# Kernel tuning notes

Measured on AMD Instinct MI355X. Metric: run time of the kernel, lower is better.

## Reference

```python
import jax, jax.numpy as jnp
import numpy as np

B, N, C, H = 8, 4096, 768, 8
EPS = 1e-12  # F.normalize eps


def setup_inputs() -> dict:
    key = jax.random.key(0)
    ks = jax.random.split(key, 4)
    x = jax.random.normal(ks[0], (B, N, C), dtype=jnp.float32)
    w_qkv = jax.random.normal(ks[1], (3 * C, C), dtype=jnp.float32) * 0.02
    temperature = jnp.ones((H, 1, 1), dtype=jnp.float32)
    w_proj = jax.random.normal(ks[2], (C, C), dtype=jnp.float32) * 0.02
    b_proj = jnp.zeros((C,), dtype=jnp.float32)
    return {"x": x, "w_qkv": w_qkv, "temperature": temperature,
            "w_proj": w_proj, "b_proj": b_proj}


def _l2norm(t):
    # F.normalize(t, dim=-1): t / max(||t||_2, eps)
    n = jnp.sqrt(jnp.sum(t * t, axis=-1, keepdims=True))
    return t / jnp.maximum(n, EPS)


def reference(x, w_qkv, temperature, w_proj, b_proj):
    b, n, c = x.shape
    h = H
    hd = c // h
    # qkv projection: (B,N,3C) -> (3,B,H,hd,N)
    qkv = (x @ w_qkv.T).reshape(b, n, 3, h, hd)
    qkv = jnp.transpose(qkv, (2, 0, 3, 4, 1))
    q, k, v = qkv[0], qkv[1], qkv[2]          # each (B,H,hd,N)
    qn = _l2norm(q)                            # normalize over N (token) dim
    kn = _l2norm(k)
    # small per-head covariance attention: (B,H,hd,hd)
    attn = jnp.einsum('bhdn,bhen->bhde', qn, kn) * temperature
    attn = jax.nn.softmax(attn, axis=-1)
    out = jnp.einsum('bhde,bhen->bhdn', attn, v)  # (B,H,hd,N)
    out = jnp.transpose(out, (0, 3, 1, 2)).reshape(b, n, c)
    return out @ w_proj.T + b_proj
```

## Files before the change

### kernel.cpp

```cpp
#include <hip/hip_runtime.h>
#include <cstdint>
#include <cstddef>

#define B_ 8
#define N_ 4096
#define C_ 768
#define H_ 8
#define HD_ 96
#define EPSN 1e-12f
#define NS_ 4

typedef short s16x8 __attribute__((ext_vector_type(8)));
typedef short s16x4 __attribute__((ext_vector_type(4)));
typedef float f32x4 __attribute__((ext_vector_type(4)));

static __device__ __forceinline__ short f2bf(float f) {
  unsigned u = __float_as_uint(f);
  unsigned r = (u + 0x7fff + ((u >> 16) & 1)) >> 16;
  return (short)r;
}
static __device__ __forceinline__ float bf2f(unsigned short s) {
  return __uint_as_float(((unsigned)s) << 16);
}
static __device__ __forceinline__ s16x8 pack8(const float4 a, const float4 b) {
  s16x8 r;
  r[0] = f2bf(a.x); r[1] = f2bf(a.y); r[2] = f2bf(a.z); r[3] = f2bf(a.w);
  r[4] = f2bf(b.x); r[5] = f2bf(b.y); r[6] = f2bf(b.z); r[7] = f2bf(b.w);
  return r;
}

#define TSW(ch, t) ((t) ^ ((((ch) >> 2) & 7) << 3))

static __device__ __forceinline__ int swz(int s) {
  return s ^ (((s >> 7) & 3) << 3);
}

static __device__ __forceinline__ void gld16(const short* g, short* l) {
  __builtin_amdgcn_global_load_lds(
      (const __attribute__((address_space(1))) void*)g,
      (__attribute__((address_space(3))) void*)l, 16, 0, 0);
}

__global__ __launch_bounds__(256)
void xcvt(const float* __restrict__ x, short* __restrict__ xb) {
  const int n8 = (B_ * N_ * C_) / 8;
  for (int i = blockIdx.x * 256 + threadIdx.x; i < n8; i += gridDim.x * 256) {
    const float4 a = *(const float4*)(x + (size_t)i * 8);
    const float4 b = *(const float4*)(x + (size_t)i * 8 + 4);
    *(s16x8*)(xb + (size_t)i * 8) = pack8(a, b);
  }
}

__global__ __launch_bounds__(256)
void wcvt(const float* __restrict__ w, short* __restrict__ wb) {
  const int i = blockIdx.x * 256 + threadIdx.x;
  const float4 a = *(const float4*)(w + (size_t)i * 8);
  const float4 b = *(const float4*)(w + (size_t)i * 8 + 4);
  *(s16x8*)(wb + (size_t)i * 8) = pack8(a, b);
}

template<int BF>
__global__ __launch_bounds__(256)
void gram_p(const float* __restrict__ x, const short* __restrict__ xb,
            float* __restrict__ Gp) {
  const int f = blockIdx.x;
  const int xcd = f & 7;
  const int t = f >> 3;
  const int pair = t % 21;
  const int cdiv = t / 21;
  const int c = xcd + 8 * cdiv;
  const int split = c & 3;
  const int b = c >> 2;

  int rem = pair, ti = 0;
#pragma unroll
  for (int it = 0; it < 5; ++it)
    if (rem >= 6 - ti) { rem -= 6 - ti; ++ti; }
  const int tj = ti + rem;
  const int i0 = ti * 128, j0 = tj * 128;
  const bool diag = (ti == tj);

  const int tid = threadIdx.x;
  const int lane = tid & 63, wave = tid >> 6;
  const int l15 = lane & 15, quad = lane >> 4;
  const int wm = wave & 1, wn = wave >> 1;

  __shared__ __align__(16) short smem[2 * 128 * 72];
  short* At = smem;
  short* Bt = smem + 128 * 72;

  const int tg = tid >> 4;
  const int cg = tid & 15;
  const int t0 = tg * 4;
  const int c0 = cg * 4;
  const float* xbF = x + (size_t)b * N_ * C_;
  const short* xbB = xb + (size_t)b * N_ * C_;

  f32x4 acc[4][4] = {};

  const int nbeg = split * (N_ / NS_);
  const int nend = nbeg + (N_ / NS_);
  for (int n0 = nbeg; n0 < nend; n0 += 64) {
    if (BF) {
      s16x8 la[4], lb[4];
#pragma unroll
      for (int r = 0; r < 4; ++r)
        la[r] = *(const s16x8*)(xbB + (size_t)(n0 + t0 + r) * C_ + i0 + cg * 8);
      if (!diag) {
#pragma unroll
        for (int r = 0; r < 4; ++r)
          lb[r] = *(const s16x8*)(xbB + (size_t)(n0 + t0 + r) * C_ + j0 + cg * 8);
      }
      __syncthreads();
#pragma unroll
      for (int cc = 0; cc < 8; ++cc) {
        const int ch = cg * 8 + cc;
        s16x4 v;
        v[0] = la[0][cc]; v[1] = la[1][cc]; v[2] = la[2][cc]; v[3] = la[3][cc];
        *(s16x4*)&At[ch * 72 + TSW(ch, t0)] = v;
      }
      if (!diag) {
#pragma unroll
        for (int cc = 0; cc < 8; ++cc) {
          const int ch = cg * 8 + cc;
          s16x4 v;
          v[0] = lb[0][cc]; v[1] = lb[1][cc]; v[2] = lb[2][cc]; v[3] = lb[3][cc];
          *(s16x4*)&Bt[ch * 72 + TSW(ch, t0)] = v;
        }
      }
      __syncthreads();
    } else {
      float4 la[2][4], lb[2][4];
#pragma unroll
      for (int q = 0; q < 2; ++q)
#pragma unroll
        for (int r = 0; r < 4; ++r)
          la[q][r] = *(const float4*)(xbF + (size_t)(n0 + t0 + r) * C_ + i0 + c0 + q * 64);
      if (!diag) {
#pragma unroll
        for (int q = 0; q < 2; ++q)
#pragma unroll
          for (int r = 0; r < 4; ++r)
            lb[q][r] = *(const float4*)(xbF + (size_t)(n0 + t0 + r) * C_ + j0 + c0 + q * 64);
      }
      __syncthreads();
#pragma unroll
      for (int q = 0; q < 2; ++q)
#pragma unroll
        for (int cc = 0; cc < 4; ++cc) {
          const int ch = c0 + q * 64 + cc;
          s16x4 v;
          v[0] = f2bf(((const float*)&la[q][0])[cc]);
          v[1] = f2bf(((const float*)&la[q][1])[cc]);
          v[2] = f2bf(((const float*)&la[q][2])[cc]);
          v[3] = f2bf(((const float*)&la[q][3])[cc]);
          *(s16x4*)&At[ch * 72 + TSW(ch, t0)] = v;
        }
      if (!diag) {
#pragma unroll
        for (int q = 0; q < 2; ++q)
#pragma unroll
          for (int cc = 0; cc < 4; ++cc) {
            const int ch = c0 + q * 64 + cc;
            s16x4 v;
            v[0] = f2bf(((const float*)&lb[q][0])[cc]);
            v[1] = f2bf(((const float*)&lb[q][1])[cc]);
            v[2] = f2bf(((const float*)&lb[q][2])[cc]);
            v[3] = f2bf(((const float*)&lb[q][3])[cc]);
            *(s16x4*)&Bt[ch * 72 + TSW(ch, t0)] = v;
          }
      }
      __syncthreads();
    }
    const short* Bre = diag ? At : Bt;
#pragma unroll
    for (int ks = 0; ks < 64; ks += 32) {
      s16x8 af[4], bfr[4];
#pragma unroll
      for (int mi = 0; mi < 4; ++mi) {
        const int ch = wm * 64 + mi * 16 + l15;
        af[mi] = *(const s16x8*)&At[ch * 72 + TSW(ch, ks + quad * 8)];
      }
#pragma unroll
      for (int ni = 0; ni < 4; ++ni) {
        const int ch = wn * 64 + ni * 16 + l15;
        bfr[ni] = *(const s16x8*)&Bre[ch * 72 + TSW(ch, ks + quad * 8)];
      }
#pragma unroll
      for (int ni = 0; ni < 4; ++ni)
#pragma unroll
        for (int mi = 0; mi < 4; ++mi)
          acc[mi][ni] = __builtin_amdgcn_mfma_f32_16x16x32_bf16(af[mi], bfr[ni], acc[mi][ni], 0, 0, 0);
    }
  }

  float* Gpb = Gp + (((size_t)b * 21 + pair) * NS_ + split) * (128 * 128);
#pragma unroll
  for (int mi = 0; mi < 4; ++mi)
#pragma unroll
    for (int ni = 0; ni < 4; ++ni) {
      const int ii = wm * 64 + mi * 16 + quad * 4;
      const int jj = wn * 64 + ni * 16 + l15;
#pragma unroll
      for (int r = 0; r < 4; ++r)
        Gpb[(ii + r) * 128 + jj] = acc[mi][ni][r];
    }
}

__global__ __launch_bounds__(256)
void gram_red(const float* __restrict__ Gp, short* __restrict__ G) {
  const int pair = blockIdx.x;
  int rem = pair, ti = 0;
#pragma unroll
  for (int it = 0; it < 5; ++it)
    if (rem >= 6 - ti) { rem -= 6 - ti; ++ti; }
  const int tj = ti + rem;
  const int b = blockIdx.y;
  const int i0 = ti * 128, j0 = tj * 128;
  const bool diag = (ti == tj);
  const int tid = threadIdx.x;

  __shared__ short Ts[128 * 137];

  const float4* P = (const float4*)(Gp + (((size_t)b * 21 + pair) * NS_) * (128 * 128));
  short* Gb = G + (size_t)b * C_ * C_;

#pragma unroll
  for (int it = 0; it < 16; ++it) {
    const int q = tid + it * 256;
    const int row = q >> 5;
    const int c4 = q & 31;
    float4 v = P[q];
    const float4 v1 = P[q + 4096];
    const float4 v2 = P[q + 8192];
    const float4 v3 = P[q + 12288];
    v.x += v1.x + v2.x + v3.x;
    v.y += v1.y + v2.y + v3.y;
    v.z += v1.z + v2.z + v3.z;
    v.w += v1.w + v2.w + v3.w;
    s16x4 sv;
    sv[0] = f2bf(v.x); sv[1] = f2bf(v.y); sv[2] = f2bf(v.z); sv[3] = f2bf(v.w);
    *(s16x4*)&Gb[(size_t)(i0 + row) * C_ + j0 + c4 * 4] = sv;
    if (!diag) {
#pragma unroll
      for (int c = 0; c < 4; ++c)
        Ts[(c4 * 4 + c) * 137 + row] = sv[c];
    }
  }
  if (!diag) {
    __syncthreads();
#pragma unroll
    for (int p = 0; p < 8; ++p) {
      const int id = tid + p * 256;
      const int j = id >> 4, cs = (id & 15) * 8;
      *(s16x8*)&Gb[(size_t)(j0 + j) * C_ + i0 + cs] = *(const s16x8*)&Ts[j * 137 + cs];
    }
  }
}

__global__ __launch_bounds__(256)
void gemm_nt_bf(const short* __restrict__ A, const short* __restrict__ Bb,
                short* __restrict__ Out, size_t sB, size_t sO) {
  const int z = blockIdx.z;
  const int n0 = blockIdx.x * 128;
  const int m0 = blockIdx.y * 128;
  const int tid = threadIdx.x;
  const int lane = tid & 63, wave = tid >> 6;
  const int l15 = lane & 15, quad = lane >> 4;
  const int wm = wave & 1, wn = wave >> 1;

  __shared__ __align__(16) short As[2][128 * 32];
  __shared__ __align__(16) short Bs[2][128 * 32];

  const short* asrc[2]; const short* bsrc[2];
  int doff[2];
#pragma unroll
  for (int cc = 0; cc < 2; ++cc) {
    const int P = wave * 1024 + cc * 512 + lane * 8;
    const int L = swz(P);
    const int row = L >> 5, col = L & 31;
    asrc[cc] = A + (size_t)(m0 + row) * C_ + col;
    bsrc[cc] = Bb + (size_t)z * sB + (size_t)(n0 + row) * C_ + col;
    doff[cc] = wave * 1024 + cc * 512;
  }

  f32x4 acc[4][4] = {};

#pragma unroll
  for (int cc = 0; cc < 2; ++cc) {
    gld16(asrc[cc], &As[0][doff[cc]]);
    gld16(bsrc[cc], &Bs[0][doff[cc]]);
  }
#pragma unroll
  for (int cc = 0; cc < 2; ++cc) {
    gld16(asrc[cc] + 32, &As[1][doff[cc]]);
    gld16(bsrc[cc] + 32, &Bs[1][doff[cc]]);
  }

  int cur = 0;
  const int NT = C_ / 32;
  for (int t = 0; t < NT; ++t) {
    if (t < NT - 1) asm volatile("s_waitcnt vmcnt(4)" ::: "memory");
    else            asm volatile("s_waitcnt vmcnt(0)" ::: "memory");
    __builtin_amdgcn_sched_barrier(0);
    __builtin_amdgcn_s_barrier();
    s16x8 af[4];
#pragma unroll
    for (int mi = 0; mi < 4; ++mi)
      af[mi] = *(const s16x8*)&As[cur][swz((wm * 64 + mi * 16 + l15) * 32 + quad * 8)];
    __builtin_amdgcn_s_setprio(1);
#pragma unroll
    for (int ni = 0; ni < 4; ++ni) {
      const s16x8 bf = *(const s16x8*)&Bs[cur][swz((wn * 64 + ni * 16 + l15) * 32 + quad * 8)];
#pragma unroll
      for (int mi = 0; mi < 4; ++mi)
        acc[mi][ni] = __builtin_amdgcn_mfma_f32_16x16x32_bf16(af[mi], bf, acc[mi][ni], 0, 0, 0);
    }
    __builtin_amdgcn_s_setprio(0);
    __builtin_amdgcn_sched_barrier(0);
    __builtin_amdgcn_s_barrier();
    __builtin_amdgcn_sched_barrier(0);
    if (t + 2 < NT) {
      const int nx = (t + 2) * 32;
#pragma unroll
      for (int cc = 0; cc < 2; ++cc) {
        gld16(asrc[cc] + nx, &As[cur][doff[cc]]);
        gld16(bsrc[cc] + nx, &Bs[cur][doff[cc]]);
      }
    }
    cur ^= 1;
  }

  short* ob = Out + (size_t)z * sO;
#pragma unroll
  for (int mi = 0; mi < 4; ++mi) {
    const int m = m0 + wm * 64 + mi * 16 + quad * 4;
#pragma unroll
    for (int ni = 0; ni < 4; ++ni) {
      const int n = n0 + wn * 64 + ni * 16 + l15;
#pragma unroll
      for (int r = 0; r < 4; ++r)
        ob[(size_t)(m + r) * C_ + n] = f2bf(acc[mi][ni][r]);
    }
  }
}

__global__ __launch_bounds__(256)
void gemm_fb(const float* __restrict__ A, const short* __restrict__ Bb,
             short* __restrict__ Out, size_t sB, size_t sO) {
  const int z = blockIdx.z;
  const int n0 = blockIdx.x * 128;
  const int m0 = blockIdx.y * 128;
  const int tid = threadIdx.x;
  const int lane = tid & 63, wave = tid >> 6;
  const int l15 = lane & 15, quad = lane >> 4;
  const int wm = wave & 1, wn = wave >> 1;

  __shared__ __align__(16) short As[2][128 * 40];
  __shared__ __align__(16) short Bs[2][128 * 32];

  const int ar = tid >> 1;
  const int ak = (tid & 1) * 16;
  const float* ap = A + (size_t)(m0 + ar) * C_ + ak;

  const short* bsrc[2];
  int doff[2];
#pragma unroll
  for (int cc = 0; cc < 2; ++cc) {
    const int P = wave * 1024 + cc * 512 + lane * 8;
    const int L = swz(P);
    bsrc[cc] = Bb + (size_t)z * sB + (size_t)(n0 + (L >> 5)) * C_ + (L & 31);
    doff[cc] = wave * 1024 + cc * 512;
  }

  f32x4 acc[4][4] = {};

  {
    const float4 a0 = *(const float4*)(ap + 0);
    const float4 a1 = *(const float4*)(ap + 4);
    const float4 a2 = *(const float4*)(ap + 8);
    const float4 a3 = *(const float4*)(ap + 12);
#pragma unroll
    for (int cc = 0; cc < 2; ++cc) gld16(bsrc[cc], &Bs[0][doff[cc]]);
    *(s16x8*)&As[0][ar * 40 + ak]     = pack8(a0, a1);
    *(s16x8*)&As[0][ar * 40 + ak + 8] = pack8(a2, a3);
  }
  __syncthreads();
  int cur = 0;
  for (int k0 = 0; k0 < C_; k0 += 32) {
    const int nx = k0 + 32;
    float4 a0, a1, a2, a3;
    if (nx < C_) {
      a0 = *(const float4*)(ap + nx + 0);
      a1 = *(const float4*)(ap + nx + 4);
      a2 = *(const float4*)(ap + nx + 8);
      a3 = *(const float4*)(ap + nx + 12);
#pragma unroll
      for (int cc = 0; cc < 2; ++cc) gld16(bsrc[cc] + nx, &Bs[cur ^ 1][doff[cc]]);
    }
    s16x8 af[4];
#pragma unroll
    for (int mi = 0; mi < 4; ++mi)
      af[mi] = *(const s16x8*)&As[cur][(wm * 64 + mi * 16 + l15) * 40 + quad * 8];
#pragma unroll
    for (int ni = 0; ni < 4; ++ni) {
      const s16x8 bf = *(const s16x8*)&Bs[cur][swz((wn * 64 + ni * 16 + l15) * 32 + quad * 8)];
#pragma unroll
      for (int mi = 0; mi < 4; ++mi)
        acc[mi][ni] = __builtin_amdgcn_mfma_f32_16x16x32_bf16(af[mi], bf, acc[mi][ni], 0, 0, 0);
    }
    if (nx < C_) {
      *(s16x8*)&As[cur ^ 1][ar * 40 + ak]     = pack8(a0, a1);
      *(s16x8*)&As[cur ^ 1][ar * 40 + ak + 8] = pack8(a2, a3);
    }
    __syncthreads();
    cur ^= 1;
  }

  short* ob = Out + (size_t)z * sO;
#pragma unroll
  for (int mi = 0; mi < 4; ++mi) {
    const int m = m0 + wm * 64 + mi * 16 + quad * 4;
#pragma unroll
    for (int ni = 0; ni < 4; ++ni) {
      const int n = n0 + wn * 64 + ni * 16 + l15;
#pragma unroll
      for (int r = 0; r < 4; ++r)
        ob[(size_t)(m + r) * C_ + n] = f2bf(acc[mi][ni][r]);
    }
  }
}

__global__ __launch_bounds__(256)
void row_norms(const short* __restrict__ Y, const float* __restrict__ w_qkv,
               float* __restrict__ norms) {
  const int b = blockIdx.y;
  const int m = blockIdx.x * 4 + (threadIdx.x >> 6);
  const int lane = threadIdx.x & 63;
  const short* y = Y + ((size_t)b * 1536 + m) * C_;
  const float* w = w_qkv + (size_t)m * C_;
  float s = 0.f;
#pragma unroll
  for (int j = 0; j < 3; ++j) {
    const int o = j * 256 + lane * 4;
    const s16x4 yv = *(const s16x4*)(y + o);
    const float4 wv = *(const float4*)(w + o);
    s += bf2f((unsigned short)yv[0]) * wv.x + bf2f((unsigned short)yv[1]) * wv.y +
         bf2f((unsigned short)yv[2]) * wv.z + bf2f((unsigned short)yv[3]) * wv.w;
  }
#pragma unroll
  for (int o = 32; o > 0; o >>= 1) s += __shfl_xor(s, o);
  if (lane == 0) {
    int idx;
    if (m < 768) idx = (b * 8 + m / 96) * 96 + (m % 96);
    else { const int mm = m - 768; idx = B_ * H_ * 96 + (b * 8 + mm / 96) * 96 + (mm % 96); }
    norms[idx] = s;
  }
}

__global__ __launch_bounds__(512)
void s_attn(const short* __restrict__ Y, const short* __restrict__ wb,
            const float* __restrict__ norms, const float* __restrict__ temp,
            float* __restrict__ S) {
  const int bh = blockIdx.x;
  const int b = bh >> 3, h = bh & 7;
  const int tid = threadIdx.x;
  const int lane = tid & 63, wave = tid >> 6;
  const int l15 = lane & 15, quad = lane >> 4;

  __shared__ __align__(16) float Sf[96 * 97];
  __shared__ float qsc[96], ksc[96];
  short* Ys = (short*)Sf;
  short* Ks = (short*)Sf + 96 * 72;

  if (tid < 96)
    qsc[tid] = temp[h] / fmaxf(sqrtf(norms[bh * 96 + tid]), EPSN);
  else if (tid < 192)
    ksc[tid - 96] = 1.0f / fmaxf(sqrtf(norms[B_ * H_ * 96 + bh * 96 + (tid - 96)]), EPSN);

  const short* yb = Y + ((size_t)b * 1536 + h * 96) * C_;
  const short* kb = wb + (size_t)(768 + h * 96) * C_;

  int dts[5], ets[5];
#pragma unroll
  for (int j = 0; j < 5; ++j) {
    const int t = j * 8 + wave;
    dts[j] = t / 6; ets[j] = t % 6;
  }

  f32x4 sc[5] = {};
  const int r0 = tid >> 3, c80 = (tid & 7) * 8;
  const int id1 = tid + 512;
  const int r1 = id1 >> 3, c81 = (id1 & 7) * 8;
  for (int k0 = 0; k0 < C_; k0 += 64) {
    s16x8 yv0, kv0, yv1, kv1;
    yv0 = *(const s16x8*)(yb + (size_t)r0 * C_ + k0 + c80);
    kv0 = *(const s16x8*)(kb + (size_t)r0 * C_ + k0 + c80);
    if (tid < 256) {
      yv1 = *(const s16x8*)(yb + (size_t)r1 * C_ + k0 + c81);
      kv1 = *(const s16x8*)(kb + (size_t)r1 * C_ + k0 + c81);
    }
    __syncthreads();
    *(s16x8*)&Ys[r0 * 72 + c80] = yv0;
    *(s16x8*)&Ks[r0 * 72 + c80] = kv0;
    if (tid < 256) {
      *(s16x8*)&Ys[r1 * 72 + c81] = yv1;
      *(s16x8*)&Ks[r1 * 72 + c81] = kv1;
    }
    __syncthreads();
#pragma unroll
    for (int j = 0; j < 5; ++j) {
      const int t = j * 8 + wave;
      if (t < 36) {
#pragma unroll
        for (int kk = 0; kk < 64; kk += 32) {
          const s16x8 a  = *(const s16x8*)&Ys[(dts[j] * 16 + l15) * 72 + kk + quad * 8];
          const s16x8 bb = *(const s16x8*)&Ks[(ets[j] * 16 + l15) * 72 + kk + quad * 8];
          sc[j] = __builtin_amdgcn_mfma_f32_16x16x32_bf16(a, bb, sc[j], 0, 0, 0);
        }
      }
    }
  }
  __syncthreads();
#pragma unroll
  for (int j = 0; j < 5; ++j) {
    const int t = j * 8 + wave;
    if (t < 36) {
      const int e = ets[j] * 16 + l15;
      const float kf = ksc[e];
#pragma unroll
      for (int r = 0; r < 4; ++r) {
        const int d = dts[j] * 16 + quad * 4 + r;
        Sf[d * 97 + e] = sc[j][r] * qsc[d] * kf;
      }
    }
  }
  __syncthreads();
  float* Sb = S + (size_t)bh * (HD_ * HD_);
  for (int rr = 0; rr < 12; ++rr) {
    const int d = wave * 12 + rr;
    const float v0 = Sf[d * 97 + lane];
    const float v1 = (lane < 32) ? Sf[d * 97 + 64 + lane] : -1e30f;
    float mx = fmaxf(v0, v1);
#pragma unroll
    for (int o = 32; o > 0; o >>= 1) mx = fmaxf(mx, __shfl_xor(mx, o));
    const float e0 = __expf(v0 - mx);
    const float e1 = (lane < 32) ? __expf(v1 - mx) : 0.0f;
    float sum = e0 + e1;
#pragma unroll
    for (int o = 32; o > 0; o >>= 1) sum += __shfl_xor(sum, o);
    const float inv = 1.0f / sum;
    Sb[d * 96 + lane] = e0 * inv;
    if (lane < 32) Sb[d * 96 + 64 + lane] = e1 * inv;
  }
}

__global__ __launch_bounds__(256)
void av_gemm(const float* __restrict__ S, const float* __restrict__ w_qkv,
             short* __restrict__ AVt) {
  const int bh = blockIdx.x;
  const int b = bh >> 3, h = bh & 7;
  const int ct = blockIdx.y * 64;
  const int tid = threadIdx.x;
  __shared__ float at[96 * 97];
  __shared__ float wv[96 * 64];
  const float* Sb = S + (size_t)bh * (HD_ * HD_);
  for (int i = tid; i < 96 * 96; i += 256)
    at[(i / 96) * 97 + (i % 96)] = Sb[i];
  for (int i = tid; i < 96 * 64; i += 256) {
    const int e = i >> 6, c = i & 63;
    wv[e * 64 + c] = w_qkv[(size_t)(2 * C_ + h * 96 + e) * C_ + ct + c];
  }
  __syncthreads();
  const int d0 = (tid >> 4) * 6;
  const int c0 = (tid & 15) * 4;
  float acc[6][4] = {};
  for (int e = 0; e < 96; ++e) {
    const float4 bv = *(const float4*)&wv[e * 64 + c0];
    float aa[6];
#pragma unroll
    for (int i = 0; i < 6; ++i) aa[i] = at[(d0 + i) * 97 + e];
#pragma unroll
    for (int i = 0; i < 6; ++i) {
      acc[i][0] += aa[i] * bv.x; acc[i][1] += aa[i] * bv.y;
      acc[i][2] += aa[i] * bv.z; acc[i][3] += aa[i] * bv.w;
    }
  }
  short* AVb = AVt + (size_t)b * C_ * C_;
#pragma unroll
  for (int i = 0; i < 6; ++i)
#pragma unroll
    for (int j = 0; j < 4; ++j)
      AVb[(size_t)(ct + c0 + j) * C_ + h * 96 + d0 + i] = f2bf(acc[i][j]);
}

__global__ __launch_bounds__(256)
void gemm_xm_bf(const short* __restrict__ xb, const short* __restrict__ Mb,
                const float* __restrict__ bias, float* __restrict__ out) {
  const int f = blockIdx.x;
  const int xcd = f & 7;
  const int t6 = f >> 3;
  const int j6 = t6 % 6;
  const int sdiv = t6 / 6;
  const int s = xcd + 8 * sdiv;
  const int z = s >> 5;
  const int n0 = j6 * 128;
  const int m0 = (s & 31) * 128;
  const int tid = threadIdx.x;
  const int lane = tid & 63;
  const int wave = tid >> 6;
  const int l15 = lane & 15;
  const int quad = lane >> 4;
  const int wm = wave & 1;
  const int wn = wave >> 1;

  __shared__ __align__(16) short As[2][128 * 32];
  __shared__ __align__(16) short Bs[2][128 * 32];

  const short* asrc[2]; const short* bsrc[2];
  int doff[2];
#pragma unroll
  for (int cc = 0; cc < 2; ++cc) {
    const int P = wave * 1024 + cc * 512 + lane * 8;
    const int L = swz(P);
    const int row = L >> 5, col = L & 31;
    asrc[cc] = xb + ((size_t)z * N_ + m0 + row) * C_ + col;
    bsrc[cc] = Mb + (size_t)z * C_ * C_ + (size_t)(n0 + row) * C_ + col;
    doff[cc] = wave * 1024 + cc * 512;
  }

  f32x4 acc[4][4] = {};

#pragma unroll
  for (int cc = 0; cc < 2; ++cc) {
    gld16(asrc[cc], &As[0][doff[cc]]);
    gld16(bsrc[cc], &Bs[0][doff[cc]]);
  }
#pragma unroll
  for (int cc = 0; cc < 2; ++cc) {
    gld16(asrc[cc] + 32, &As[1][doff[cc]]);
    gld16(bsrc[cc] + 32, &Bs[1][doff[cc]]);
  }

  int cur = 0;
  const int NT = C_ / 32;
  for (int t = 0; t < NT; ++t) {
    if (t < NT - 1) asm volatile("s_waitcnt vmcnt(4)" ::: "memory");
    else            asm volatile("s_waitcnt vmcnt(0)" ::: "memory");
    __builtin_amdgcn_sched_barrier(0);
    __builtin_amdgcn_s_barrier();
    s16x8 af[4];
#pragma unroll
    for (int mi = 0; mi < 4; ++mi)
      af[mi] = *(const s16x8*)&As[cur][swz((wm * 64 + mi * 16 + l15) * 32 + quad * 8)];
    __builtin_amdgcn_s_setprio(1);
#pragma unroll
    for (int ni = 0; ni < 4; ++ni) {
      const s16x8 bf = *(const s16x8*)&Bs[cur][swz((wn * 64 + ni * 16 + l15) * 32 + quad * 8)];
#pragma unroll
      for (int mi = 0; mi < 4; ++mi)
        acc[mi][ni] = __builtin_amdgcn_mfma_f32_16x16x32_bf16(af[mi], bf, acc[mi][ni], 0, 0, 0);
    }
    __builtin_amdgcn_s_setprio(0);
    __builtin_amdgcn_sched_barrier(0);
    __builtin_amdgcn_s_barrier();
    __builtin_amdgcn_sched_barrier(0);
    if (t + 2 < NT) {
      const int nx = (t + 2) * 32;
#pragma unroll
      for (int cc = 0; cc < 2; ++cc) {
        gld16(asrc[cc] + nx, &As[cur][doff[cc]]);
        gld16(bsrc[cc] + nx, &Bs[cur][doff[cc]]);
      }
    }
    cur ^= 1;
  }

  float bv[4];
#pragma unroll
  for (int ni = 0; ni < 4; ++ni) bv[ni] = bias[n0 + wn * 64 + ni * 16 + l15];
#pragma unroll
  for (int mi = 0; mi < 4; ++mi) {
    const int m = m0 + wm * 64 + mi * 16 + quad * 4;
#pragma unroll
    for (int ni = 0; ni < 4; ++ni) {
      const int n = n0 + wn * 64 + ni * 16 + l15;
      float* dst = out + ((size_t)z * N_ + m) * C_ + n;
#pragma unroll
      for (int r = 0; r < 4; ++r)
        dst[(size_t)r * C_] = acc[mi][ni][r] + bv[ni];
    }
  }
}

__global__ __launch_bounds__(256)
void gemm_xm_f32(const float* __restrict__ x, const short* __restrict__ Mb,
                 const float* __restrict__ bias, float* __restrict__ out) {
  const int f = blockIdx.x;
  const int xcd = f & 7;
  const int t = f >> 3;
  const int j6 = t % 6;
  const int sdiv = t / 6;
  const int s = xcd + 8 * sdiv;
  const int z = s >> 5;
  const int n0 = j6 * 128;
  const int m0 = (s & 31) * 128;
  const int tid = threadIdx.x;
  const int lane = tid & 63;
  const int wave = tid >> 6;
  const int l15 = lane & 15;
  const int quad = lane >> 4;
  const int wm = wave & 1;
  const int wn = wave >> 1;

  __shared__ __align__(16) short As[128 * 40];
  __shared__ __align__(16) short Bs[128 * 40];

  const int ar = tid >> 1;
  const int ak = (tid & 1) * 16;
  const float* xp = x + ((size_t)z * N_ + m0 + ar) * C_ + ak;
  const short* mp = Mb + (size_t)z * C_ * C_ + (size_t)(n0 + ar) * C_ + ak;

  f32x4 acc[4][4] = {};

  for (int k0 = 0; k0 < C_; k0 += 32) {
    const float4 a0 = *(const float4*)(xp + k0 + 0);
    const float4 a1 = *(const float4*)(xp + k0 + 4);
    const float4 a2 = *(const float4*)(xp + k0 + 8);
    const float4 a3 = *(const float4*)(xp + k0 + 12);
    const s16x8 b0 = *(const s16x8*)(mp + k0 + 0);
    const s16x8 b1 = *(const s16x8*)(mp + k0 + 8);
    __syncthreads();
    *(s16x8*)&As[ar * 40 + ak]     = pack8(a0, a1);
    *(s16x8*)&As[ar * 40 + ak + 8] = pack8(a2, a3);
    *(s16x8*)&Bs[ar * 40 + ak]     = b0;
    *(s16x8*)&Bs[ar * 40 + ak + 8] = b1;
    __syncthreads();
    s16x8 af[4];
#pragma unroll
    for (int mi = 0; mi < 4; ++mi)
      af[mi] = *(const s16x8*)&As[(wm * 64 + mi * 16 + l15) * 40 + quad * 8];
#pragma unroll
    for (int ni = 0; ni < 4; ++ni) {
      const s16x8 bf = *(const s16x8*)&Bs[(wn * 64 + ni * 16 + l15) * 40 + quad * 8];
#pragma unroll
      for (int mi = 0; mi < 4; ++mi)
        acc[mi][ni] = __builtin_amdgcn_mfma_f32_16x16x32_bf16(af[mi], bf, acc[mi][ni], 0, 0, 0);
    }
  }

  float bv[4];
#pragma unroll
  for (int ni = 0; ni < 4; ++ni) bv[ni] = bias[n0 + wn * 64 + ni * 16 + l15];
#pragma unroll
  for (int mi = 0; mi < 4; ++mi) {
    const int m = m0 + wm * 64 + mi * 16 + quad * 4;
#pragma unroll
    for (int ni = 0; ni < 4; ++ni) {
      const int n = n0 + wn * 64 + ni * 16 + l15;
      float* dst = out + ((size_t)z * N_ + m) * C_ + n;
#pragma unroll
      for (int r = 0; r < 4; ++r)
        dst[(size_t)r * C_] = acc[mi][ni][r] + bv[ni];
    }
  }
}

extern "C" void kernel_launch(void* const* d_in, const int* in_sizes, int n_in,
                              void* d_out, int out_size, void* d_ws, size_t ws_size,
                              hipStream_t stream) {
  const float* x      = (const float*)d_in[0];
  const float* w_qkv  = (const float*)d_in[1];
  const float* temp   = (const float*)d_in[2];
  const float* w_proj = (const float*)d_in[3];
  const float* b_proj = (const float*)d_in[4];
  float* out = (float*)d_out;

  char* base = (char*)d_ws;
  float* S     = (float*)base;
  float* norms = (float*)(base + 2359296);
  short* G     = (short*)(base + 2408448);
  short* AVt   = G;
  short* Mb    = (short*)(base + 11845632);
  short* Y     = (short*)(base + 21282816);
  short* wb    = (short*)(base + 11845632);

  const size_t need1 = 55885824 + 50331648;
  const size_t need2 = 40157184 + 50331648;
  const int tier = (ws_size >= need1) ? 1 : (ws_size >= need2) ? 2 : 3;

  float* Gp = (tier == 2) ? (float*)(base + 40157184) : (float*)(base + 11845632);
  short* xb = (tier == 1) ? (short*)(base + 55885824)
            : (tier == 2) ? (short*)(base + 40157184) : nullptr;

  if (tier == 1) {
    xcvt<<<3072, 256, 0, stream>>>(x, xb);
    gram_p<1><<<21 * NS_ * B_, 256, 0, stream>>>(x, xb, Gp);
  } else {
    gram_p<0><<<21 * NS_ * B_, 256, 0, stream>>>(x, xb ? xb : (const short*)G, Gp);
  }

  gram_red<<<dim3(21, B_), 256, 0, stream>>>(Gp, G);

  if (tier == 2) xcvt<<<3072, 256, 0, stream>>>(x, xb);

  wcvt<<<576, 256, 0, stream>>>(w_qkv, wb);

  gemm_nt_bf<<<dim3(C_ / 128, 1536 / 128, B_), 256, 0, stream>>>(
      wb, G, Y, (size_t)C_ * C_, (size_t)1536 * C_);

  row_norms<<<dim3(1536 / 4, B_), 256, 0, stream>>>(Y, w_qkv, norms);

  s_attn<<<B_ * H_, 512, 0, stream>>>(Y, wb, norms, temp, S);

  av_gemm<<<dim3(B_ * H_, C_ / 64), 256, 0, stream>>>(S, w_qkv, AVt);

  gemm_fb<<<dim3(C_ / 128, C_ / 128, B_), 256, 0, stream>>>(
      w_proj, AVt, Mb, (size_t)C_ * C_, (size_t)C_ * C_);

  if (tier == 3)
    gemm_xm_f32<<<C_ / 128 * (N_ / 128) * B_, 256, 0, stream>>>(x, Mb, b_proj, out);
  else
    gemm_xm_bf<<<C_ / 128 * (N_ / 128) * B_, 256, 0, stream>>>(xb, Mb, b_proj, out);
}
```

Before: 399.0 us.

## Fuse bf16 conversion of x into gram kernel; triple-buffer GEMM LDS pipelines

The separate xcvt pass is dropped on the tier-1 path. The gram kernel now reads fp32 x directly, and its diagonal tiles write the bf16 copy of x as a side effect. The GEMM kernels move from two to three LDS stages, which removes one barrier per k-step by issuing the next prefetch into a buffer that is no longer being read. This saves a full read and write pass over x and some synchronisation, in exchange for more LDS per block and more fp32 traffic into the gram kernel.

Result: slower. 422.6 us (+5.9%).

```diff
diff --git a/kernel.cpp b/kernel.cpp
--- a/kernel.cpp
+++ b/kernel.cpp
@@ -59,9 +59,9 @@
   *(s16x8*)(wb + (size_t)i * 8) = pack8(a, b);
 }
 
-template<int BF>
-__global__ __launch_bounds__(256)
-void gram_p(const float* __restrict__ x, const short* __restrict__ xb,
+template<int MODE>
+__global__ __launch_bounds__(256)
+void gram_p(const float* __restrict__ x, short* __restrict__ xbw,
             float* __restrict__ Gp) {
   const int f = blockIdx.x;
   const int xcd = f & 7;
@@ -94,84 +94,71 @@
   const int t0 = tg * 4;
   const int c0 = cg * 4;
   const float* xbF = x + (size_t)b * N_ * C_;
-  const short* xbB = xb + (size_t)b * N_ * C_;
+  short* xbO = xbw + (size_t)b * N_ * C_;
 
   f32x4 acc[4][4] = {};
 
   const int nbeg = split * (N_ / NS_);
   const int nend = nbeg + (N_ / NS_);
   for (int n0 = nbeg; n0 < nend; n0 += 64) {
-    if (BF) {
-      s16x8 la[4], lb[4];
+    float4 la[2][4], lb[2][4];
+#pragma unroll
+    for (int q = 0; q < 2; ++q)
 #pragma unroll
       for (int r = 0; r < 4; ++r)
-        la[r] = *(const s16x8*)(xbB + (size_t)(n0 + t0 + r) * C_ + i0 + cg * 8);
-      if (!diag) {
+        la[q][r] = *(const float4*)(xbF + (size_t)(n0 + t0 + r) * C_ + i0 + c0 + q * 64);
+    if (!diag) {
+#pragma unroll
+      for (int q = 0; q < 2; ++q)
 #pragma unroll
         for (int r = 0; r < 4; ++r)
-          lb[r] = *(const s16x8*)(xbB + (size_t)(n0 + t0 + r) * C_ + j0 + cg * 8);
-      }
-      __syncthreads();
-#pragma unroll
-      for (int cc = 0; cc < 8; ++cc) {
-        const int ch = cg * 8 + cc;
+          lb[q][r] = *(const float4*)(xbF + (size_t)(n0 + t0 + r) * C_ + j0 + c0 + q * 64);
+    }
+    short cb[2][4][4];
+#pragma unroll
+    for (int q = 0; q < 2; ++q)
+#pragma unroll
+      for (int r = 0; r < 4; ++r)
+#pragma unroll
+        for (int cc = 0; cc < 4; ++cc)
+          cb[q][r][cc] = f2bf(((const float*)&la[q][r])[cc]);
+    if (MODE == 2 && diag) {
+#pragma unroll
+      for (int q = 0; q < 2; ++q)
+#pragma unroll
+        for (int r = 0; r < 4; ++r) {
+          s16x4 sv;
+          sv[0] = cb[q][r][0]; sv[1] = cb[q][r][1];
+          sv[2] = cb[q][r][2]; sv[3] = cb[q][r][3];
+          *(s16x4*)&xbO[(size_t)(n0 + t0 + r) * C_ + i0 + c0 + q * 64] = sv;
+        }
+    }
+    __syncthreads();
+#pragma unroll
+    for (int q = 0; q < 2; ++q)
+#pragma unroll
+      for (int cc = 0; cc < 4; ++cc) {
+        const int ch = c0 + q * 64 + cc;
         s16x4 v;
-        v[0] = la[0][cc]; v[1] = la[1][cc]; v[2] = la[2][cc]; v[3] = la[3][cc];
+        v[0] = cb[q][0][cc]; v[1] = cb[q][1][cc];
+        v[2] = cb[q][2][cc]; v[3] = cb[q][3][cc];
         *(s16x4*)&At[ch * 72 + TSW(ch, t0)] = v;
       }
-      if (!diag) {
-#pragma unroll
-        for (int cc = 0; cc < 8; ++cc) {
-          const int ch = cg * 8 + cc;
-          s16x4 v;
-          v[0] = lb[0][cc]; v[1] = lb[1][cc]; v[2] = lb[2][cc]; v[3] = lb[3][cc];
-          *(s16x4*)&Bt[ch * 72 + TSW(ch, t0)] = v;
-        }
-      }
-      __syncthreads();
-    } else {
-      float4 la[2][4], lb[2][4];
-#pragma unroll
-      for (int q = 0; q < 2; ++q)
-#pragma unroll
-        for (int r = 0; r < 4; ++r)
-          la[q][r] = *(const float4*)(xbF + (size_t)(n0 + t0 + r) * C_ + i0 + c0 + q * 64);
-      if (!diag) {
-#pragma unroll
-        for (int q = 0; q < 2; ++q)
-#pragma unroll
-          for (int r = 0; r < 4; ++r)
-            lb[q][r] = *(const float4*)(xbF + (size_t)(n0 + t0 + r) * C_ + j0 + c0 + q * 64);
-      }
-      __syncthreads();
+    if (!diag) {
 #pragma unroll
       for (int q = 0; q < 2; ++q)
 #pragma unroll
         for (int cc = 0; cc < 4; ++cc) {
           const int ch = c0 + q * 64 + cc;
           s16x4 v;
-          v[0] = f2bf(((const float*)&la[q][0])[cc]);
-          v[1] = f2bf(((const float*)&la[q][1])[cc]);
-          v[2] = f2bf(((const float*)&la[q][2])[cc]);
-          v[3] = f2bf(((const float*)&la[q][3])[cc]);
-          *(s16x4*)&At[ch * 72 + TSW(ch, t0)] = v;
+          v[0] = f2bf(((const float*)&lb[q][0])[cc]);
+          v[1] = f2bf(((const float*)&lb[q][1])[cc]);
+          v[2] = f2bf(((const float*)&lb[q][2])[cc]);
+          v[3] = f2bf(((const float*)&lb[q][3])[cc]);
+          *(s16x4*)&Bt[ch * 72 + TSW(ch, t0)] = v;
         }
-      if (!diag) {
-#pragma unroll
-        for (int q = 0; q < 2; ++q)
-#pragma unroll
-          for (int cc = 0; cc < 4; ++cc) {
-            const int ch = c0 + q * 64 + cc;
-            s16x4 v;
-            v[0] = f2bf(((const float*)&lb[q][0])[cc]);
-            v[1] = f2bf(((const float*)&lb[q][1])[cc]);
-            v[2] = f2bf(((const float*)&lb[q][2])[cc]);
-            v[3] = f2bf(((const float*)&lb[q][3])[cc]);
-            *(s16x4*)&Bt[ch * 72 + TSW(ch, t0)] = v;
-          }
-      }
-      __syncthreads();
-    }
+    }
+    __syncthreads();
     const short* Bre = diag ? At : Bt;
 #pragma unroll
     for (int ks = 0; ks < 64; ks += 32) {
@@ -269,8 +256,8 @@
   const int l15 = lane & 15, quad = lane >> 4;
   const int wm = wave & 1, wn = wave >> 1;
 
-  __shared__ __align__(16) short As[2][128 * 32];
-  __shared__ __align__(16) short Bs[2][128 * 32];
+  __shared__ __align__(16) short As[3][128 * 32];
+  __shared__ __align__(16) short Bs[3][128 * 32];
 
   const short* asrc[2]; const short* bsrc[2];
   int doff[2];
@@ -302,33 +289,31 @@
   for (int t = 0; t < NT; ++t) {
     if (t < NT - 1) asm volatile("s_waitcnt vmcnt(4)" ::: "memory");
     else            asm volatile("s_waitcnt vmcnt(0)" ::: "memory");
-    __builtin_amdgcn_sched_barrier(0);
-    __builtin_amdgcn_s_barrier();
-    s16x8 af[4];
-#pragma unroll
-    for (int mi = 0; mi < 4; ++mi)
-      af[mi] = *(const s16x8*)&As[cur][swz((wm * 64 + mi * 16 + l15) * 32 + quad * 8)];
-    __builtin_amdgcn_s_setprio(1);
-#pragma unroll
-    for (int ni = 0; ni < 4; ++ni) {
-      const s16x8 bf = *(const s16x8*)&Bs[cur][swz((wn * 64 + ni * 16 + l15) * 32 + quad * 8)];
-#pragma unroll
-      for (int mi = 0; mi < 4; ++mi)
-        acc[mi][ni] = __builtin_amdgcn_mfma_f32_16x16x32_bf16(af[mi], bf, acc[mi][ni], 0, 0, 0);
-    }
-    __builtin_amdgcn_s_setprio(0);
-    __builtin_amdgcn_sched_barrier(0);
     __builtin_amdgcn_s_barrier();
     __builtin_amdgcn_sched_barrier(0);
     if (t + 2 < NT) {
       const int nx = (t + 2) * 32;
+      const int pb = (cur >= 1) ? cur - 1 : 2;
 #pragma unroll
       for (int cc = 0; cc < 2; ++cc) {
-        gld16(asrc[cc] + nx, &As[cur][doff[cc]]);
-        gld16(bsrc[cc] + nx, &Bs[cur][doff[cc]]);
+        gld16(asrc[cc] + nx, &As[pb][doff[cc]]);
+        gld16(bsrc[cc] + nx, &Bs[pb][doff[cc]]);
       }
     }
-    cur ^= 1;
+    s16x8 af[4];
+#pragma unroll
+    for (int mi = 0; mi < 4; ++mi)
+      af[mi] = *(const s16x8*)&As[cur][swz((wm * 64 + mi * 16 + l15) * 32 + quad * 8)];
+    __builtin_amdgcn_s_setprio(1);
+#pragma unroll
+    for (int ni = 0; ni < 4; ++ni) {
+      const s16x8 bf = *(const s16x8*)&Bs[cur][swz((wn * 64 + ni * 16 + l15) * 32 + quad * 8)];
+#pragma unroll
+      for (int mi = 0; mi < 4; ++mi)
+        acc[mi][ni] = __builtin_amdgcn_mfma_f32_16x16x32_bf16(af[mi], bf, acc[mi][ni], 0, 0, 0);
+    }
+    __builtin_amdgcn_s_setprio(0);
+    cur = (cur + 1 == 3) ? 0 : cur + 1;
   }
 
   short* ob = Out + (size_t)z * sO;
@@ -614,8 +599,8 @@
   const int wm = wave & 1;
   const int wn = wave >> 1;
 
-  __shared__ __align__(16) short As[2][128 * 32];
-  __shared__ __align__(16) short Bs[2][128 * 32];
+  __shared__ __align__(16) short As[3][128 * 32];
+  __shared__ __align__(16) short Bs[3][128 * 32];
 
   const short* asrc[2]; const short* bsrc[2];
   int doff[2];
@@ -647,33 +632,31 @@
   for (int t = 0; t < NT; ++t) {
     if (t < NT - 1) asm volatile("s_waitcnt vmcnt(4)" ::: "memory");
     else            asm volatile("s_waitcnt vmcnt(0)" ::: "memory");
-    __builtin_amdgcn_sched_barrier(0);
-    __builtin_amdgcn_s_barrier();
-    s16x8 af[4];
-#pragma unroll
-    for (int mi = 0; mi < 4; ++mi)
-      af[mi] = *(const s16x8*)&As[cur][swz((wm * 64 + mi * 16 + l15) * 32 + quad * 8)];
-    __builtin_amdgcn_s_setprio(1);
-#pragma unroll
-    for (int ni = 0; ni < 4; ++ni) {
-      const s16x8 bf = *(const s16x8*)&Bs[cur][swz((wn * 64 + ni * 16 + l15) * 32 + quad * 8)];
-#pragma unroll
-      for (int mi = 0; mi < 4; ++mi)
-        acc[mi][ni] = __builtin_amdgcn_mfma_f32_16x16x32_bf16(af[mi], bf, acc[mi][ni], 0, 0, 0);
-    }
-    __builtin_amdgcn_s_setprio(0);
-    __builtin_amdgcn_sched_barrier(0);
     __builtin_amdgcn_s_barrier();
     __builtin_amdgcn_sched_barrier(0);
     if (t + 2 < NT) {
       const int nx = (t + 2) * 32;
+      const int pb = (cur >= 1) ? cur - 1 : 2;
 #pragma unroll
       for (int cc = 0; cc < 2; ++cc) {
-        gld16(asrc[cc] + nx, &As[cur][doff[cc]]);
-        gld16(bsrc[cc] + nx, &Bs[cur][doff[cc]]);
+        gld16(asrc[cc] + nx, &As[pb][doff[cc]]);
+        gld16(bsrc[cc] + nx, &Bs[pb][doff[cc]]);
       }
     }
-    cur ^= 1;
+    s16x8 af[4];
+#pragma unroll
+    for (int mi = 0; mi < 4; ++mi)
+      af[mi] = *(const s16x8*)&As[cur][swz((wm * 64 + mi * 16 + l15) * 32 + quad * 8)];
+    __builtin_amdgcn_s_setprio(1);
+#pragma unroll
+    for (int ni = 0; ni < 4; ++ni) {
+      const s16x8 bf = *(const s16x8*)&Bs[cur][swz((wn * 64 + ni * 16 + l15) * 32 + quad * 8)];
+#pragma unroll
+      for (int mi = 0; mi < 4; ++mi)
+        acc[mi][ni] = __builtin_amdgcn_mfma_f32_16x16x32_bf16(af[mi], bf, acc[mi][ni], 0, 0, 0);
+    }
+    __builtin_amdgcn_s_setprio(0);
+    cur = (cur + 1 == 3) ? 0 : cur + 1;
   }
 
   float bv[4];
@@ -794,10 +777,9 @@
             : (tier == 2) ? (short*)(base + 40157184) : nullptr;
 
   if (tier == 1) {
-    xcvt<<<3072, 256, 0, stream>>>(x, xb);
-    gram_p<1><<<21 * NS_ * B_, 256, 0, stream>>>(x, xb, Gp);
+    gram_p<2><<<21 * NS_ * B_, 256, 0, stream>>>(x, xb, Gp);
   } else {
-    gram_p<0><<<21 * NS_ * B_, 256, 0, stream>>>(x, xb ? xb : (const short*)G, Gp);
+    gram_p<0><<<21 * NS_ * B_, 256, 0, stream>>>(x, (short*)G, Gp);
   }
 
   gram_red<<<dim3(21, B_), 256, 0, stream>>>(Gp, G);
```
